# Kernel tuning notes

Measured on AMD Instinct MI355X. Metric: run time of the kernel, lower is better.

The kernel has to match this reference:

```python
import jax, jax.numpy as jnp
import numpy as np

N_NODES = 100000
N_EDGES = 1600000
NODE_DIM = 32
MSG_DIM = 32
COORD_DIM = 3
FF_HALF = 4  # FourierLayer(1, 8) -> coeff [1, 4]


def silu(x):
    return x * jax.nn.sigmoid(x)


def setup_inputs() -> dict:
    key = jax.random.key(0)
    ks = jax.random.split(key, 16)
    s = lambda fan_in: 1.0 / np.sqrt(fan_in)
    edge_in = 2 * NODE_DIM + 2 * FF_HALF  # 72
    node_in = MSG_DIM + NODE_DIM          # 64
    return {
        "coord": jax.random.normal(ks[0], (N_NODES, COORD_DIM), jnp.float32),
        "node_feat": jax.random.normal(ks[1], (N_NODES, NODE_DIM), jnp.float32),
        "edge_index": jax.random.randint(ks[2], (2, N_EDGES), 0, N_NODES, jnp.int64 if jax.config.jax_enable_x64 else jnp.int32),
        "ff_coeff": jax.random.normal(ks[3], (1, FF_HALF), jnp.float32),  # sigma=1.0
        "ew1": jax.random.uniform(ks[4], (edge_in, MSG_DIM), jnp.float32, -s(edge_in), s(edge_in)),
        "eb1": jax.random.uniform(ks[5], (MSG_DIM,), jnp.float32, -s(edge_in), s(edge_in)),
        "ew2": jax.random.uniform(ks[6], (MSG_DIM, MSG_DIM), jnp.float32, -s(MSG_DIM), s(MSG_DIM)),
        "eb2": jax.random.uniform(ks[7], (MSG_DIM,), jnp.float32, -s(MSG_DIM), s(MSG_DIM)),
        "cw1": jax.random.uniform(ks[8], (MSG_DIM, MSG_DIM), jnp.float32, -s(MSG_DIM), s(MSG_DIM)),
        "cb1": jax.random.uniform(ks[9], (MSG_DIM,), jnp.float32, -s(MSG_DIM), s(MSG_DIM)),
        "cw2": jax.random.uniform(ks[10], (MSG_DIM, 1), jnp.float32, -s(MSG_DIM), s(MSG_DIM)),  # bias-free last coord layer
        "nw1": jax.random.uniform(ks[11], (node_in, MSG_DIM), jnp.float32, -s(node_in), s(node_in)),
        "nb1": jax.random.uniform(ks[12], (MSG_DIM,), jnp.float32, -s(node_in), s(node_in)),
        "nw2": jax.random.uniform(ks[13], (MSG_DIM, NODE_DIM), jnp.float32, -s(MSG_DIM), s(MSG_DIM)),
        "nb2": jax.random.uniform(ks[14], (NODE_DIM,), jnp.float32, -s(MSG_DIM), s(MSG_DIM)),
    }


def reference(coord, node_feat, edge_index, ff_coeff, ew1, eb1, ew2, eb2,
              cw1, cb1, cw2, nw1, nb1, nw2, nb2):
    n = coord.shape[0]
    idx_i, idx_j = edge_index[0], edge_index[1]
    # coord2radial (sparse, normalize=False)
    coord_diff = coord[idx_i] - coord[idx_j]                 # [E, 3]
    radial = jnp.sum(coord_diff * coord_diff, axis=1, keepdims=True)  # [E, 1]
    # Fourier radial features (ffr=True): ff1(radial) -> [E, 8]
    x_proj = (2.0 * jnp.pi) * (radial @ ff_coeff)            # [E, 4]
    ff = jnp.concatenate([jnp.cos(x_proj), jnp.sin(x_proj)], axis=-1)  # [E, 8]
    # edge MLP
    edge_in = jnp.concatenate([node_feat[idx_i], node_feat[idx_j], ff], axis=1)  # [E, 72]
    m = silu(edge_in @ ew1 + eb1)
    m = silu(m @ ew2 + eb2)                                  # [E, M]
    # coord model: per-edge scalar weight on coord_diff, mean-aggregated to nodes
    w = silu(m @ cw1 + cb1) @ cw2                            # [E, 1]
    trans = coord_diff * w                                   # [E, 3]
    agg_c = jax.ops.segment_sum(trans, idx_i, num_segments=n)
    counts = jax.ops.segment_sum(jnp.ones((trans.shape[0],), trans.dtype), idx_i, num_segments=n)
    coord_out = coord + agg_c / jnp.clip(counts, 1.0)[:, None]
    # node model: sum-aggregated messages, residual
    agg_h = jax.ops.segment_sum(m, idx_i, num_segments=n)    # [N, M]
    h = silu(jnp.concatenate([node_feat, agg_h], axis=1) @ nw1 + nb1)
    h = h @ nw2 + nb2
    node_out = node_feat + h                                 # is_residual=True
    return node_out, coord_out
```

## Files before the change

kernel.cpp:

```cpp
#include <hip/hip_runtime.h>
#include <math.h>

__device__ __forceinline__ float silu_f(float x) {
    return x / (1.0f + __expf(-x));
}

__device__ __forceinline__ void sincos_2pi_rev(float rev, float& s, float& c) {
#if __has_builtin(__builtin_amdgcn_sinf) && __has_builtin(__builtin_amdgcn_cosf)
    const float fr = rev - floorf(rev);
    s = __builtin_amdgcn_sinf(fr);
    c = __builtin_amdgcn_cosf(fr);
#else
    const float xp = 6.2831853071795864769f * rev;
    s = sinf(xp); c = cosf(xp);
#endif
}

__global__ __launch_bounds__(256) void egc_proj(
    const float* __restrict__ node_feat,
    const float* __restrict__ ew1, const float* __restrict__ eb1,
    float* __restrict__ Pi, float* __restrict__ Pj, int N)
{
    const int tid = threadIdx.x;
    const int l32 = tid & 31;
    const int n = blockIdx.x * 8 + (tid >> 5);
    if (n >= N) return;

    const float nf = node_feat[(size_t)n * 32 + l32];
    float pi = eb1[l32];
    float pj = 0.0f;
    #pragma unroll
    for (int k = 0; k < 32; ++k) {
        const float b = __shfl(nf, k, 32);
        pi = fmaf(b, ew1[k * 32 + l32], pi);
        pj = fmaf(b, ew1[(32 + k) * 32 + l32], pj);
    }
    Pi[(size_t)n * 32 + l32] = pi;
    Pj[(size_t)n * 32 + l32] = pj;
}

__global__ __launch_bounds__(256) void egc_hist(
    const int* __restrict__ idx_i, int* __restrict__ counts, int E)
{
    const int e = blockIdx.x * 256 + threadIdx.x;
    if (e < E) atomicAdd(&counts[idx_i[e]], 1);
}

__global__ __launch_bounds__(1024) void egc_scan(
    const int* __restrict__ counts, int* __restrict__ row_start,
    int* __restrict__ cursor, int N)
{
    __shared__ int wsum[16];
    __shared__ int carry_s;
    const int tid = threadIdx.x;
    const int lane = tid & 63, wid = tid >> 6;
    if (tid == 0) carry_s = 0;
    __syncthreads();
    for (int base = 0; base < N; base += 4096) {
        const int i0 = base + tid * 4;
        int v0 = 0, v1 = 0, v2 = 0, v3 = 0;
        if (i0 + 3 < N) {
            const int4 q = *reinterpret_cast<const int4*>(counts + i0);
            v0 = q.x; v1 = q.y; v2 = q.z; v3 = q.w;
        } else {
            if (i0 + 0 < N) v0 = counts[i0 + 0];
            if (i0 + 1 < N) v1 = counts[i0 + 1];
            if (i0 + 2 < N) v2 = counts[i0 + 2];
        }
        const int p1 = v0, p2 = v0 + v1, p3 = v0 + v1 + v2, tot = p3 + v3;
        int incl = tot;
        #pragma unroll
        for (int off = 1; off < 64; off <<= 1) {
            int v = __shfl_up(incl, off, 64);
            if (lane >= off) incl += v;
        }
        if (lane == 63) wsum[wid] = incl;
        __syncthreads();
        if (wid == 0) {
            int v = (lane < 16) ? wsum[lane] : 0;
            int s = v;
            #pragma unroll
            for (int off = 1; off < 16; off <<= 1) {
                int t = __shfl_up(s, off, 64);
                if (lane >= off) s += t;
            }
            if (lane < 16) wsum[lane] = s - v;
        }
        __syncthreads();
        const int carry = carry_s;
        const int tb = carry + wsum[wid] + incl - tot;
        if (i0 + 0 < N) { row_start[i0 + 0] = tb;      cursor[i0 + 0] = tb; }
        if (i0 + 1 < N) { row_start[i0 + 1] = tb + p1; cursor[i0 + 1] = tb + p1; }
        if (i0 + 2 < N) { row_start[i0 + 2] = tb + p2; cursor[i0 + 2] = tb + p2; }
        if (i0 + 3 < N) { row_start[i0 + 3] = tb + p3; cursor[i0 + 3] = tb + p3; }
        __syncthreads();
        if (tid == 1023) carry_s = carry + wsum[15] + incl;
        __syncthreads();
    }
    if (tid == 0) row_start[N] = carry_s;
}

__global__ __launch_bounds__(256) void egc_scatter(
    const int* __restrict__ idx_i, int* __restrict__ cursor,
    int* __restrict__ eord, int E)
{
    const int e = blockIdx.x * 256 + threadIdx.x;
    if (e >= E) return;
    const int slot = atomicAdd(&cursor[idx_i[e]], 1);
    eord[slot] = e;
}

__global__ __launch_bounds__(256) void egc_edge_proj(
    const float* __restrict__ coord,
    const int*   __restrict__ edge_index,
    const float* __restrict__ ff_coeff,
    const float* __restrict__ Pi, const float* __restrict__ Pj,
    const float* __restrict__ ew1,
    const float* __restrict__ ew2, const float* __restrict__ eb2,
    const float* __restrict__ cw1, const float* __restrict__ cb1,
    const float* __restrict__ cw2,
    float* __restrict__ m_buf,
    float* __restrict__ trans4,
    int E)
{
    const int e = blockIdx.x * 256 + threadIdx.x;
    if (e >= E) return;

    const int i = edge_index[e];
    const int j = edge_index[E + e];

    const float cix = coord[3*(size_t)i+0], ciy = coord[3*(size_t)i+1], ciz = coord[3*(size_t)i+2];
    const float cjx = coord[3*(size_t)j+0], cjy = coord[3*(size_t)j+1], cjz = coord[3*(size_t)j+2];
    const float cdx = cix - cjx, cdy = ciy - cjy, cdz = ciz - cjz;
    const float radial = cdx*cdx + cdy*cdy + cdz*cdz;

    float ff[8];
    #pragma unroll
    for (int k = 0; k < 4; ++k) {
        float s, c;
        sincos_2pi_rev(radial * ff_coeff[k], s, c);
        ff[k]     = c;
        ff[4 + k] = s;
    }

    float acc[32];
    {
        const float4* a4 = reinterpret_cast<const float4*>(Pi + (size_t)i * 32);
        const float4* b4 = reinterpret_cast<const float4*>(Pj + (size_t)j * 32);
        #pragma unroll
        for (int q = 0; q < 8; ++q) {
            const float4 x = a4[q], y = b4[q];
            acc[4*q+0] = x.x + y.x;
            acc[4*q+1] = x.y + y.y;
            acc[4*q+2] = x.z + y.z;
            acc[4*q+3] = x.w + y.w;
        }
    }
    #pragma unroll
    for (int k = 0; k < 8; ++k) {
        const float* wr = ew1 + (64 + k) * 32;
        #pragma unroll
        for (int o = 0; o < 32; ++o)
            acc[o] = fmaf(ff[k], wr[o], acc[o]);
    }

    float m1[32];
    #pragma unroll
    for (int o = 0; o < 32; ++o) m1[o] = silu_f(acc[o]);

    float m[32];
    #pragma unroll
    for (int o = 0; o < 32; ++o) m[o] = eb2[o];
    #pragma unroll
    for (int h = 0; h < 32; ++h) {
        #pragma unroll
        for (int o = 0; o < 32; ++o)
            m[o] = fmaf(m1[h], ew2[h*32 + o], m[o]);
    }
    #pragma unroll
    for (int o = 0; o < 32; ++o) m[o] = silu_f(m[o]);

    float4* mb = reinterpret_cast<float4*>(m_buf + (size_t)e * 32);
    #pragma unroll
    for (int q = 0; q < 8; ++q) {
        float4 v;
        v.x = m[4*q+0]; v.y = m[4*q+1]; v.z = m[4*q+2]; v.w = m[4*q+3];
        mb[q] = v;
    }

    float c1[32];
    #pragma unroll
    for (int o = 0; o < 32; ++o) c1[o] = cb1[o];
    #pragma unroll
    for (int h = 0; h < 32; ++h) {
        #pragma unroll
        for (int o = 0; o < 32; ++o)
            c1[o] = fmaf(m[h], cw1[h*32 + o], c1[o]);
    }
    float w = 0.0f;
    #pragma unroll
    for (int o = 0; o < 32; ++o) w += silu_f(c1[o]) * cw2[o];

    float4 t; t.x = cdx * w; t.y = cdy * w; t.z = cdz * w; t.w = 0.0f;
    *reinterpret_cast<float4*>(trans4 + (size_t)e * 4) = t;
}

__global__ __launch_bounds__(256) void egc_edge_full(
    const float* __restrict__ coord,
    const float* __restrict__ node_feat,
    const int*   __restrict__ edge_index,
    const float* __restrict__ ff_coeff,
    const float* __restrict__ ew1, const float* __restrict__ eb1,
    const float* __restrict__ ew2, const float* __restrict__ eb2,
    const float* __restrict__ cw1, const float* __restrict__ cb1,
    const float* __restrict__ cw2,
    float* __restrict__ m_buf, float* __restrict__ trans4, int E)
{
    const int e = blockIdx.x * 256 + threadIdx.x;
    if (e >= E) return;

    const int i = edge_index[e];
    const int j = edge_index[E + e];

    const float cix = coord[3*(size_t)i+0], ciy = coord[3*(size_t)i+1], ciz = coord[3*(size_t)i+2];
    const float cjx = coord[3*(size_t)j+0], cjy = coord[3*(size_t)j+1], cjz = coord[3*(size_t)j+2];
    const float cdx = cix - cjx, cdy = ciy - cjy, cdz = ciz - cjz;
    const float radial = cdx*cdx + cdy*cdy + cdz*cdz;

    float ff[8];
    #pragma unroll
    for (int k = 0; k < 4; ++k) {
        float s, c;
        sincos_2pi_rev(radial * ff_coeff[k], s, c);
        ff[k] = c; ff[4+k] = s;
    }

    float acc[32];
    #pragma unroll
    for (int o = 0; o < 32; ++o) acc[o] = eb1[o];
    {
        const float4* nfi4 = reinterpret_cast<const float4*>(node_feat + (size_t)i * 32);
        for (int q = 0; q < 8; ++q) {
            float4 v = nfi4[q];
            float xs[4] = {v.x, v.y, v.z, v.w};
            const float* wr = ew1 + q * 4 * 32;
            #pragma unroll
            for (int kk = 0; kk < 4; ++kk)
                #pragma unroll
                for (int o = 0; o < 32; ++o)
                    acc[o] = fmaf(xs[kk], wr[kk*32 + o], acc[o]);
        }
        const float4* nfj4 = reinterpret_cast<const float4*>(node_feat + (size_t)j * 32);
        for (int q = 0; q < 8; ++q) {
            float4 v = nfj4[q];
            float xs[4] = {v.x, v.y, v.z, v.w};
            const float* wr = ew1 + (32 + q * 4) * 32;
            #pragma unroll
            for (int kk = 0; kk < 4; ++kk)
                #pragma unroll
                for (int o = 0; o < 32; ++o)
                    acc[o] = fmaf(xs[kk], wr[kk*32 + o], acc[o]);
        }
        #pragma unroll
        for (int k = 0; k < 8; ++k) {
            const float* wr = ew1 + (64 + k) * 32;
            #pragma unroll
            for (int o = 0; o < 32; ++o)
                acc[o] = fmaf(ff[k], wr[o], acc[o]);
        }
    }
    float m1[32];
    #pragma unroll
    for (int o = 0; o < 32; ++o) m1[o] = silu_f(acc[o]);
    float m[32];
    #pragma unroll
    for (int o = 0; o < 32; ++o) m[o] = eb2[o];
    #pragma unroll
    for (int h = 0; h < 32; ++h)
        #pragma unroll
        for (int o = 0; o < 32; ++o)
            m[o] = fmaf(m1[h], ew2[h*32 + o], m[o]);
    #pragma unroll
    for (int o = 0; o < 32; ++o) m[o] = silu_f(m[o]);

    float4* mb = reinterpret_cast<float4*>(m_buf + (size_t)e * 32);
    #pragma unroll
    for (int q = 0; q < 8; ++q) {
        float4 v;
        v.x = m[4*q+0]; v.y = m[4*q+1]; v.z = m[4*q+2]; v.w = m[4*q+3];
        mb[q] = v;
    }

    float c1[32];
    #pragma unroll
    for (int o = 0; o < 32; ++o) c1[o] = cb1[o];
    #pragma unroll
    for (int h = 0; h < 32; ++h)
        #pragma unroll
        for (int o = 0; o < 32; ++o)
            c1[o] = fmaf(m[h], cw1[h*32 + o], c1[o]);
    float w = 0.0f;
    #pragma unroll
    for (int o = 0; o < 32; ++o) w += silu_f(c1[o]) * cw2[o];

    float4 t; t.x = cdx * w; t.y = cdy * w; t.z = cdz * w; t.w = 0.0f;
    *reinterpret_cast<float4*>(trans4 + (size_t)e * 4) = t;
}

__global__ __launch_bounds__(256) void egc_node_wave(
    const float* __restrict__ coord,
    const float* __restrict__ node_feat,
    const float* __restrict__ m_buf,
    const float* __restrict__ trans4,
    const int*   __restrict__ eord,
    const int*   __restrict__ row_start,
    const float* __restrict__ nw1, const float* __restrict__ nb1,
    const float* __restrict__ nw2, const float* __restrict__ nb2,
    float* __restrict__ out_node, float* __restrict__ out_coord, int N)
{
    const int tid = threadIdx.x;
    const int l32 = tid & 31;
    const int n = blockIdx.x * 8 + (tid >> 5);
    if (n >= N) return;

    const int rs = row_start[n];
    const int re = row_start[n + 1];

    float agg = 0.0f;
    float tr  = 0.0f;
    for (int k = rs; k < re; ++k) {
        const int e = eord[k];
        agg += m_buf[(size_t)e * 32 + l32];
        if (l32 < 3) tr += trans4[(size_t)e * 4 + l32];
    }

    const float nf = node_feat[(size_t)n * 32 + l32];

    float acc = nb1[l32];
    #pragma unroll
    for (int k = 0; k < 32; ++k)
        acc = fmaf(__shfl(nf, k, 32), nw1[k*32 + l32], acc);
    #pragma unroll
    for (int k = 0; k < 32; ++k)
        acc = fmaf(__shfl(agg, k, 32), nw1[(32+k)*32 + l32], acc);
    const float h1 = silu_f(acc);

    float h2 = nb2[l32];
    #pragma unroll
    for (int k = 0; k < 32; ++k)
        h2 = fmaf(__shfl(h1, k, 32), nw2[k*32 + l32], h2);

    out_node[(size_t)n * 32 + l32] = nf + h2;

    if (l32 < 3) {
        const float deg = (float)(re - rs);
        out_coord[(size_t)n * 3 + l32] =
            coord[(size_t)n * 3 + l32] + tr / fmaxf(deg, 1.0f);
    }
}

__global__ __launch_bounds__(256) void egc_edge_fb(
    const float* __restrict__ coord,
    const float* __restrict__ node_feat,
    const int*   __restrict__ edge_index,
    const float* __restrict__ ff_coeff,
    const float* __restrict__ ew1, const float* __restrict__ eb1,
    const float* __restrict__ ew2, const float* __restrict__ eb2,
    const float* __restrict__ cw1, const float* __restrict__ cb1,
    const float* __restrict__ cw2,
    float* __restrict__ agg_h, float* __restrict__ agg_c, float* __restrict__ counts,
    int E)
{
    const int e = blockIdx.x * 256 + threadIdx.x;
    if (e >= E) return;
    const int i = edge_index[e];
    const int j = edge_index[E + e];

    const float cix = coord[3*(size_t)i+0], ciy = coord[3*(size_t)i+1], ciz = coord[3*(size_t)i+2];
    const float cjx = coord[3*(size_t)j+0], cjy = coord[3*(size_t)j+1], cjz = coord[3*(size_t)j+2];
    const float cdx = cix - cjx, cdy = ciy - cjy, cdz = ciz - cjz;
    const float radial = cdx*cdx + cdy*cdy + cdz*cdz;

    float ff[8];
    #pragma unroll
    for (int k = 0; k < 4; ++k) {
        float s, c;
        sincos_2pi_rev(radial * ff_coeff[k], s, c);
        ff[k] = c; ff[4+k] = s;
    }
    float acc[32];
    #pragma unroll
    for (int o = 0; o < 32; ++o) acc[o] = eb1[o];
    {
        const float4* nfi4 = reinterpret_cast<const float4*>(node_feat + (size_t)i * 32);
        for (int q = 0; q < 8; ++q) {
            float4 v = nfi4[q];
            float xs[4] = {v.x, v.y, v.z, v.w};
            const float* wr = ew1 + q * 4 * 32;
            #pragma unroll
            for (int kk = 0; kk < 4; ++kk)
                #pragma unroll
                for (int o = 0; o < 32; ++o)
                    acc[o] = fmaf(xs[kk], wr[kk*32 + o], acc[o]);
        }
        const float4* nfj4 = reinterpret_cast<const float4*>(node_feat + (size_t)j * 32);
        for (int q = 0; q < 8; ++q) {
            float4 v = nfj4[q];
            float xs[4] = {v.x, v.y, v.z, v.w};
            const float* wr = ew1 + (32 + q * 4) * 32;
            #pragma unroll
            for (int kk = 0; kk < 4; ++kk)
                #pragma unroll
                for (int o = 0; o < 32; ++o)
                    acc[o] = fmaf(xs[kk], wr[kk*32 + o], acc[o]);
        }
        #pragma unroll
        for (int k = 0; k < 8; ++k) {
            const float* wr = ew1 + (64 + k) * 32;
            #pragma unroll
            for (int o = 0; o < 32; ++o)
                acc[o] = fmaf(ff[k], wr[o], acc[o]);
        }
    }
    float m1[32];
    #pragma unroll
    for (int o = 0; o < 32; ++o) m1[o] = silu_f(acc[o]);
    float m[32];
    #pragma unroll
    for (int o = 0; o < 32; ++o) m[o] = eb2[o];
    #pragma unroll
    for (int h = 0; h < 32; ++h)
        #pragma unroll
        for (int o = 0; o < 32; ++o)
            m[o] = fmaf(m1[h], ew2[h*32 + o], m[o]);
    #pragma unroll
    for (int o = 0; o < 32; ++o) m[o] = silu_f(m[o]);

    float* dst = agg_h + (size_t)i * 32;
    #pragma unroll
    for (int o = 0; o < 32; ++o) atomicAdd(&dst[o], m[o]);

    float c1[32];
    #pragma unroll
    for (int o = 0; o < 32; ++o) c1[o] = cb1[o];
    #pragma unroll
    for (int h = 0; h < 32; ++h)
        #pragma unroll
        for (int o = 0; o < 32; ++o)
            c1[o] = fmaf(m[h], cw1[h*32 + o], c1[o]);
    float w = 0.0f;
    #pragma unroll
    for (int o = 0; o < 32; ++o) w += silu_f(c1[o]) * cw2[o];

    atomicAdd(&agg_c[(size_t)i*3 + 0], cdx * w);
    atomicAdd(&agg_c[(size_t)i*3 + 1], cdy * w);
    atomicAdd(&agg_c[(size_t)i*3 + 2], cdz * w);
    atomicAdd(&counts[i], 1.0f);
}

__global__ __launch_bounds__(256) void egc_node_fb(
    const float* __restrict__ coord,
    const float* __restrict__ node_feat,
    const float* __restrict__ agg_h,
    const float* __restrict__ agg_c,
    const float* __restrict__ counts,
    const float* __restrict__ nw1, const float* __restrict__ nb1,
    const float* __restrict__ nw2, const float* __restrict__ nb2,
    float* __restrict__ out_node, float* __restrict__ out_coord, int N)
{
    const int tid = threadIdx.x;
    const int l32 = tid & 31;
    const int n = blockIdx.x * 8 + (tid >> 5);
    if (n >= N) return;

    const float nf  = node_feat[(size_t)n * 32 + l32];
    const float agg = agg_h[(size_t)n * 32 + l32];

    float acc = nb1[l32];
    #pragma unroll
    for (int k = 0; k < 32; ++k)
        acc = fmaf(__shfl(nf, k, 32), nw1[k*32 + l32], acc);
    #pragma unroll
    for (int k = 0; k < 32; ++k)
        acc = fmaf(__shfl(agg, k, 32), nw1[(32+k)*32 + l32], acc);
    const float h1 = silu_f(acc);

    float h2 = nb2[l32];
    #pragma unroll
    for (int k = 0; k < 32; ++k)
        h2 = fmaf(__shfl(h1, k, 32), nw2[k*32 + l32], h2);

    out_node[(size_t)n * 32 + l32] = nf + h2;

    if (l32 < 3) {
        const float cnt = fmaxf(counts[n], 1.0f);
        out_coord[(size_t)n * 3 + l32] =
            coord[(size_t)n * 3 + l32] + agg_c[(size_t)n * 3 + l32] / cnt;
    }
}


extern "C" void kernel_launch(void* const* d_in, const int* in_sizes, int n_in,
                              void* d_out, int out_size, void* d_ws, size_t ws_size,
                              hipStream_t stream) {
    const float* coord     = (const float*)d_in[0];
    const float* node_feat = (const float*)d_in[1];
    const int*   edge_index= (const int*)  d_in[2];
    const float* ff_coeff  = (const float*)d_in[3];
    const float* ew1 = (const float*)d_in[4];
    const float* eb1 = (const float*)d_in[5];
    const float* ew2 = (const float*)d_in[6];
    const float* eb2 = (const float*)d_in[7];
    const float* cw1 = (const float*)d_in[8];
    const float* cb1 = (const float*)d_in[9];
    const float* cw2 = (const float*)d_in[10];
    const float* nw1 = (const float*)d_in[11];
    const float* nb1 = (const float*)d_in[12];
    const float* nw2 = (const float*)d_in[13];
    const float* nb2 = (const float*)d_in[14];

    const int N = in_sizes[0] / 3;
    const int E = in_sizes[2] / 2;

    float* out_node  = (float*)d_out;
    float* out_coord = out_node + (size_t)N * 32;

    const size_t m_off   = 0;
    const size_t t_off   = m_off + (size_t)E * 32;
    const size_t eo_off  = t_off + (size_t)E * 4;
    const size_t cnt_off = eo_off + (size_t)E;
    const size_t cur_off = cnt_off + (size_t)N;
    const size_t rs_off  = cur_off + (size_t)N;
    const size_t pi_off  = (rs_off + (size_t)N + 1 + 3) & ~(size_t)3;
    const size_t pj_off  = pi_off + (size_t)N * 32;
    const size_t need_A  = (pj_off + (size_t)N * 32) * 4 + 256;
    const size_t need_B  = (rs_off + (size_t)N + 1) * 4 + 256;

    if (ws_size >= need_B) {
        float* m_buf     = (float*)d_ws + m_off;
        float* trans4    = (float*)d_ws + t_off;
        int*   eord      = (int*)d_ws + eo_off;
        int*   counts    = (int*)d_ws + cnt_off;
        int*   cursor    = (int*)d_ws + cur_off;
        int*   row_start = (int*)d_ws + rs_off;

        hipMemsetAsync(counts, 0, (size_t)N * sizeof(int), stream);

        egc_hist<<<(E + 255) / 256, 256, 0, stream>>>(edge_index, counts, E);
        egc_scan<<<1, 1024, 0, stream>>>(counts, row_start, cursor, N);
        egc_scatter<<<(E + 255) / 256, 256, 0, stream>>>(edge_index, cursor, eord, E);

        if (ws_size >= need_A) {
            float* Pi = (float*)d_ws + pi_off;
            float* Pj = (float*)d_ws + pj_off;
            egc_proj<<<(N + 7) / 8, 256, 0, stream>>>(node_feat, ew1, eb1, Pi, Pj, N);
            egc_edge_proj<<<(E + 255) / 256, 256, 0, stream>>>(
                coord, edge_index, ff_coeff, Pi, Pj,
                ew1, ew2, eb2, cw1, cb1, cw2, m_buf, trans4, E);
        } else {
            egc_edge_full<<<(E + 255) / 256, 256, 0, stream>>>(
                coord, node_feat, edge_index, ff_coeff,
                ew1, eb1, ew2, eb2, cw1, cb1, cw2, m_buf, trans4, E);
        }

        egc_node_wave<<<(N + 7) / 8, 256, 0, stream>>>(
            coord, node_feat, m_buf, trans4, eord, row_start,
            nw1, nb1, nw2, nb2, out_node, out_coord, N);
    } else {
        float* agg_h  = (float*)d_ws;
        float* agg_c  = agg_h + (size_t)N * 32;
        float* counts = agg_c + (size_t)N * 3;
        hipMemsetAsync(d_ws, 0, (size_t)N * 36 * sizeof(float), stream);

        egc_edge_fb<<<(E + 255) / 256, 256, 0, stream>>>(
            coord, node_feat, edge_index, ff_coeff,
            ew1, eb1, ew2, eb2, cw1, cb1, cw2,
            agg_h, agg_c, counts, E);

        egc_node_fb<<<(N + 7) / 8, 256, 0, stream>>>(
            coord, node_feat, agg_h, agg_c, counts,
            nw1, nb1, nw2, nb2, out_node, out_coord, N);
    }
}
```

Baseline: 742.4 us.

## Fuse CSR scatter into edge kernel, shrink trans buffer, add nontemporal accesses

Removes the separate egc_scatter launch by taking the cursor slot with an atomic inside the edge MLP kernel and writing eord there. The coordinate-translation buffer shrinks from four floats to three per edge, and m_buf/trans are written and read with nontemporal hints. The histogram kernel now reads four indices per thread, and the node gather loop is unrolled by two. These cut launches and memory traffic; the atomic adds latency to the edge kernel, and unaligned 3-float scalar stores may coalesce less well.

```diff
diff --git a/kernel.cpp b/kernel.cpp
--- a/kernel.cpp
+++ b/kernel.cpp
@@ -16,6 +16,16 @@
 #endif
 }
 
+typedef float v4f __attribute__((ext_vector_type(4)));
+
+__device__ __forceinline__ void nt_store4(float* p, float a, float b, float c, float d) {
+    v4f v = {a, b, c, d};
+    __builtin_nontemporal_store(v, reinterpret_cast<v4f*>(p));
+}
+__device__ __forceinline__ float nt_loadf(const float* p) {
+    return __builtin_nontemporal_load(p);
+}
+
 __global__ __launch_bounds__(256) void egc_proj(
     const float* __restrict__ node_feat,
     const float* __restrict__ ew1, const float* __restrict__ eb1,
@@ -42,8 +52,17 @@
 __global__ __launch_bounds__(256) void egc_hist(
     const int* __restrict__ idx_i, int* __restrict__ counts, int E)
 {
-    const int e = blockIdx.x * 256 + threadIdx.x;
-    if (e < E) atomicAdd(&counts[idx_i[e]], 1);
+    const int t = blockIdx.x * 256 + threadIdx.x;
+    const int e0 = t * 4;
+    if (e0 + 3 < E) {
+        const int4 q = *reinterpret_cast<const int4*>(idx_i + e0);
+        atomicAdd(&counts[q.x], 1);
+        atomicAdd(&counts[q.y], 1);
+        atomicAdd(&counts[q.z], 1);
+        atomicAdd(&counts[q.w], 1);
+    } else {
+        for (int e = e0; e < E; ++e) atomicAdd(&counts[idx_i[e]], 1);
+    }
 }
 
 __global__ __launch_bounds__(1024) void egc_scan(
@@ -100,16 +119,6 @@
     if (tid == 0) row_start[N] = carry_s;
 }
 
-__global__ __launch_bounds__(256) void egc_scatter(
-    const int* __restrict__ idx_i, int* __restrict__ cursor,
-    int* __restrict__ eord, int E)
-{
-    const int e = blockIdx.x * 256 + threadIdx.x;
-    if (e >= E) return;
-    const int slot = atomicAdd(&cursor[idx_i[e]], 1);
-    eord[slot] = e;
-}
-
 __global__ __launch_bounds__(256) void egc_edge_proj(
     const float* __restrict__ coord,
     const int*   __restrict__ edge_index,
@@ -119,8 +128,10 @@
     const float* __restrict__ ew2, const float* __restrict__ eb2,
     const float* __restrict__ cw1, const float* __restrict__ cb1,
     const float* __restrict__ cw2,
+    int*   __restrict__ cursor,
     float* __restrict__ m_buf,
-    float* __restrict__ trans4,
+    float* __restrict__ trans3,
+    int*   __restrict__ eord,
     int E)
 {
     const int e = blockIdx.x * 256 + threadIdx.x;
@@ -128,6 +139,7 @@
 
     const int i = edge_index[e];
     const int j = edge_index[E + e];
+    const int slot = atomicAdd(&cursor[i], 1);
 
     const float cix = coord[3*(size_t)i+0], ciy = coord[3*(size_t)i+1], ciz = coord[3*(size_t)i+2];
     const float cjx = coord[3*(size_t)j+0], cjy = coord[3*(size_t)j+1], cjz = coord[3*(size_t)j+2];
@@ -180,13 +192,10 @@
     #pragma unroll
     for (int o = 0; o < 32; ++o) m[o] = silu_f(m[o]);
 
-    float4* mb = reinterpret_cast<float4*>(m_buf + (size_t)e * 32);
-    #pragma unroll
-    for (int q = 0; q < 8; ++q) {
-        float4 v;
-        v.x = m[4*q+0]; v.y = m[4*q+1]; v.z = m[4*q+2]; v.w = m[4*q+3];
-        mb[q] = v;
-    }
+    float* mb = m_buf + (size_t)e * 32;
+    #pragma unroll
+    for (int q = 0; q < 8; ++q)
+        nt_store4(mb + 4*q, m[4*q+0], m[4*q+1], m[4*q+2], m[4*q+3]);
 
     float c1[32];
     #pragma unroll
@@ -201,8 +210,12 @@
     #pragma unroll
     for (int o = 0; o < 32; ++o) w += silu_f(c1[o]) * cw2[o];
 
-    float4 t; t.x = cdx * w; t.y = cdy * w; t.z = cdz * w; t.w = 0.0f;
-    *reinterpret_cast<float4*>(trans4 + (size_t)e * 4) = t;
+    float* tp = trans3 + (size_t)e * 3;
+    __builtin_nontemporal_store(cdx * w, tp + 0);
+    __builtin_nontemporal_store(cdy * w, tp + 1);
+    __builtin_nontemporal_store(cdz * w, tp + 2);
+
+    eord[slot] = e;
 }
 
 __global__ __launch_bounds__(256) void egc_edge_full(
@@ -214,13 +227,16 @@
     const float* __restrict__ ew2, const float* __restrict__ eb2,
     const float* __restrict__ cw1, const float* __restrict__ cb1,
     const float* __restrict__ cw2,
-    float* __restrict__ m_buf, float* __restrict__ trans4, int E)
+    int* __restrict__ cursor,
+    float* __restrict__ m_buf, float* __restrict__ trans3,
+    int* __restrict__ eord, int E)
 {
     const int e = blockIdx.x * 256 + threadIdx.x;
     if (e >= E) return;
 
     const int i = edge_index[e];
     const int j = edge_index[E + e];
+    const int slot = atomicAdd(&cursor[i], 1);
 
     const float cix = coord[3*(size_t)i+0], ciy = coord[3*(size_t)i+1], ciz = coord[3*(size_t)i+2];
     const float cjx = coord[3*(size_t)j+0], cjy = coord[3*(size_t)j+1], cjz = coord[3*(size_t)j+2];
@@ -283,13 +299,10 @@
     #pragma unroll
     for (int o = 0; o < 32; ++o) m[o] = silu_f(m[o]);
 
-    float4* mb = reinterpret_cast<float4*>(m_buf + (size_t)e * 32);
-    #pragma unroll
-    for (int q = 0; q < 8; ++q) {
-        float4 v;
-        v.x = m[4*q+0]; v.y = m[4*q+1]; v.z = m[4*q+2]; v.w = m[4*q+3];
-        mb[q] = v;
-    }
+    float* mb = m_buf + (size_t)e * 32;
+    #pragma unroll
+    for (int q = 0; q < 8; ++q)
+        nt_store4(mb + 4*q, m[4*q+0], m[4*q+1], m[4*q+2], m[4*q+3]);
 
     float c1[32];
     #pragma unroll
@@ -303,15 +316,19 @@
     #pragma unroll
     for (int o = 0; o < 32; ++o) w += silu_f(c1[o]) * cw2[o];
 
-    float4 t; t.x = cdx * w; t.y = cdy * w; t.z = cdz * w; t.w = 0.0f;
-    *reinterpret_cast<float4*>(trans4 + (size_t)e * 4) = t;
+    float* tp = trans3 + (size_t)e * 3;
+    __builtin_nontemporal_store(cdx * w, tp + 0);
+    __builtin_nontemporal_store(cdy * w, tp + 1);
+    __builtin_nontemporal_store(cdz * w, tp + 2);
+
+    eord[slot] = e;
 }
 
 __global__ __launch_bounds__(256) void egc_node_wave(
     const float* __restrict__ coord,
     const float* __restrict__ node_feat,
     const float* __restrict__ m_buf,
-    const float* __restrict__ trans4,
+    const float* __restrict__ trans3,
     const int*   __restrict__ eord,
     const int*   __restrict__ row_start,
     const float* __restrict__ nw1, const float* __restrict__ nb1,
@@ -328,27 +345,38 @@
 
     float agg = 0.0f;
     float tr  = 0.0f;
-    for (int k = rs; k < re; ++k) {
-        const int e = eord[k];
-        agg += m_buf[(size_t)e * 32 + l32];
-        if (l32 < 3) tr += trans4[(size_t)e * 4 + l32];
+    int k = rs;
+    for (; k + 2 <= re; k += 2) {
+        const int e0 = eord[k];
+        const int e1 = eord[k + 1];
+        const float a0 = nt_loadf(m_buf + (size_t)e0 * 32 + l32);
+        const float a1 = nt_loadf(m_buf + (size_t)e1 * 32 + l32);
+        agg += a0 + a1;
+        if (l32 < 3)
+            tr += nt_loadf(trans3 + (size_t)e0 * 3 + l32)
+                + nt_loadf(trans3 + (size_t)e1 * 3 + l32);
+    }
+    if (k < re) {
+        const int e0 = eord[k];
+        agg += nt_loadf(m_buf + (size_t)e0 * 32 + l32);
+        if (l32 < 3) tr += nt_loadf(trans3 + (size_t)e0 * 3 + l32);
     }
 
     const float nf = node_feat[(size_t)n * 32 + l32];
 
     float acc = nb1[l32];
     #pragma unroll
-    for (int k = 0; k < 32; ++k)
-        acc = fmaf(__shfl(nf, k, 32), nw1[k*32 + l32], acc);
-    #pragma unroll
-    for (int k = 0; k < 32; ++k)
-        acc = fmaf(__shfl(agg, k, 32), nw1[(32+k)*32 + l32], acc);
+    for (int kk = 0; kk < 32; ++kk)
+        acc = fmaf(__shfl(nf, kk, 32), nw1[kk*32 + l32], acc);
+    #pragma unroll
+    for (int kk = 0; kk < 32; ++kk)
+        acc = fmaf(__shfl(agg, kk, 32), nw1[(32+kk)*32 + l32], acc);
     const float h1 = silu_f(acc);
 
     float h2 = nb2[l32];
     #pragma unroll
-    for (int k = 0; k < 32; ++k)
-        h2 = fmaf(__shfl(h1, k, 32), nw2[k*32 + l32], h2);
+    for (int kk = 0; kk < 32; ++kk)
+        h2 = fmaf(__shfl(h1, kk, 32), nw2[kk*32 + l32], h2);
 
     out_node[(size_t)n * 32 + l32] = nf + h2;
 
@@ -527,7 +555,7 @@
 
     const size_t m_off   = 0;
     const size_t t_off   = m_off + (size_t)E * 32;
-    const size_t eo_off  = t_off + (size_t)E * 4;
+    const size_t eo_off  = (t_off + (size_t)E * 3 + 3) & ~(size_t)3;
     const size_t cnt_off = eo_off + (size_t)E;
     const size_t cur_off = cnt_off + (size_t)N;
     const size_t rs_off  = cur_off + (size_t)N;
@@ -538,7 +566,7 @@
 
     if (ws_size >= need_B) {
         float* m_buf     = (float*)d_ws + m_off;
-        float* trans4    = (float*)d_ws + t_off;
+        float* trans3    = (float*)d_ws + t_off;
         int*   eord      = (int*)d_ws + eo_off;
         int*   counts    = (int*)d_ws + cnt_off;
         int*   cursor    = (int*)d_ws + cur_off;
@@ -546,9 +574,8 @@
 
         hipMemsetAsync(counts, 0, (size_t)N * sizeof(int), stream);
 
-        egc_hist<<<(E + 255) / 256, 256, 0, stream>>>(edge_index, counts, E);
+        egc_hist<<<(E / 4 + 256) / 256, 256, 0, stream>>>(edge_index, counts, E);
         egc_scan<<<1, 1024, 0, stream>>>(counts, row_start, cursor, N);
-        egc_scatter<<<(E + 255) / 256, 256, 0, stream>>>(edge_index, cursor, eord, E);
 
         if (ws_size >= need_A) {
             float* Pi = (float*)d_ws + pi_off;
@@ -556,15 +583,17 @@
             egc_proj<<<(N + 7) / 8, 256, 0, stream>>>(node_feat, ew1, eb1, Pi, Pj, N);
             egc_edge_proj<<<(E + 255) / 256, 256, 0, stream>>>(
                 coord, edge_index, ff_coeff, Pi, Pj,
-                ew1, ew2, eb2, cw1, cb1, cw2, m_buf, trans4, E);
+                ew1, ew2, eb2, cw1, cb1, cw2,
+                cursor, m_buf, trans3, eord, E);
         } else {
             egc_edge_full<<<(E + 255) / 256, 256, 0, stream>>>(
                 coord, node_feat, edge_index, ff_coeff,
-                ew1, eb1, ew2, eb2, cw1, cb1, cw2, m_buf, trans4, E);
+                ew1, eb1, ew2, eb2, cw1, cb1, cw2,
+                cursor, m_buf, trans3, eord, E);
         }
 
         egc_node_wave<<<(N + 7) / 8, 256, 0, stream>>>(
-            coord, node_feat, m_buf, trans4, eord, row_start,
+            coord, node_feat, m_buf, trans3, eord, row_start,
             nw1, nb1, nw2, nb2, out_node, out_coord, N);
     } else {
         float* agg_h  = (float*)d_ws;
```

After: 728.0 us. No clear change (-1.9%).
